# Kernel optimization log

Measured on AMD Instinct MI355X. Metric: run time of the kernel, lower is better.

## Reference

```python
import jax, jax.numpy as jnp
import numpy as np

COMPRESSION = 2

def setup_inputs() -> dict:
    key = jax.random.key(0)
    k = jax.random.split(key, 5)
    B, H, W, C, Ci = 8, 56, 56, 256, 128
    return {
        "x": jax.random.normal(k[0], (B, H, W, C), dtype=jnp.float32),
        "w_theta": jax.random.normal(k[1], (C, Ci), dtype=jnp.float32) * (2.0 / C) ** 0.5,
        "w_phi": jax.random.normal(k[2], (C, Ci), dtype=jnp.float32) * (2.0 / C) ** 0.5,
        "w_g": jax.random.normal(k[3], (C, Ci), dtype=jnp.float32) * (2.0 / C) ** 0.5,
        "w_final": jax.random.normal(k[4], (Ci, C), dtype=jnp.float32) * (2.0 / Ci) ** 0.5,
    }

def _maxpool1d(z, pool):
    # z: [B, N, Ci]; non-overlapping max pool along N (Keras MaxPool1D default stride=pool)
    B, N, Ci = z.shape
    return z[:, : (N // pool) * pool].reshape(B, N // pool, pool, Ci).max(axis=2)

def reference(x, w_theta, w_phi, w_g, w_final):
    B, H, W, C = x.shape
    Ci = w_theta.shape[1]
    N = H * W
    xf = x.reshape(B, N, C)
    # 1x1 convs == per-position matmuls
    theta = xf @ w_theta                      # [B, N, Ci]
    phi = _maxpool1d(xf @ w_phi, COMPRESSION)  # [B, N/2, Ci]
    g = _maxpool1d(xf @ w_g, COMPRESSION)      # [B, N/2, Ci]
    f = jnp.einsum('bnc,bmc->bnm', theta, phi)  # [B, N, N/2]
    f = jax.nn.softmax(f, axis=-1)
    y = jnp.einsum('bnm,bmc->bnc', f, g)        # [B, N, Ci]
    z = y @ w_final                              # [B, N, C]
    return x + z.reshape(B, H, W, C)
```

## Files before the change

### kernel.cpp

```cpp
#include <hip/hip_runtime.h>

typedef _Float16 f16x8 __attribute__((ext_vector_type(8)));
typedef _Float16 f16x4 __attribute__((ext_vector_type(4)));
typedef short s16x4 __attribute__((ext_vector_type(4)));
typedef float f32x4 __attribute__((ext_vector_type(4)));

#define MFMA_K32(a, b, c) __builtin_amdgcn_mfma_f32_16x16x32_f16(a, b, c, 0, 0, 0)
#define MFMA_BF(a, b, c)  __builtin_amdgcn_mfma_f32_16x16x16bf16_1k(a, b, c, 0, 0, 0)
#define MFMA_F16(a, b, c) __builtin_amdgcn_mfma_f32_16x16x16f16(a, b, c, 0, 0, 0)


__device__ __forceinline__ f16x8 ld8f(const float* __restrict__ p) {
    f32x4 a = *(const f32x4*)p;
    f32x4 b = *(const f32x4*)(p + 4);
    f16x8 r;
    r[0] = (_Float16)a[0]; r[1] = (_Float16)a[1];
    r[2] = (_Float16)a[2]; r[3] = (_Float16)a[3];
    r[4] = (_Float16)b[0]; r[5] = (_Float16)b[1];
    r[6] = (_Float16)b[2]; r[7] = (_Float16)b[3];
    return r;
}
__device__ __forceinline__ unsigned f2bf_rne(float f) {
    unsigned u = __float_as_uint(f);
    return (u + 0x7FFFu + ((u >> 16) & 1u)) >> 16;
}
__device__ __forceinline__ int bfpack_rtz(float lo, float hi) {
    return (int)((__float_as_uint(hi) & 0xFFFF0000u) | (__float_as_uint(lo) >> 16));
}

__global__ void k_prep(const float* __restrict__ wt, const float* __restrict__ wp,
                       const float* __restrict__ wg, const float* __restrict__ wf,
                       _Float16* __restrict__ wt_f, _Float16* __restrict__ wfT_f) {
    int i = blockIdx.x * 256 + threadIdx.x;
    int w = i >> 15, idx = i & 32767;
    if (w < 3) {
        const float* src = (w == 0) ? wt : (w == 1) ? wp : wg;
        int k = idx >> 7, n = idx & 127;
        int ct = n >> 4, tt = n & 15, kc = k >> 5, qq = (k >> 3) & 3, jj = k & 7;
        wt_f[((w * 8 + ct) * 8 + kc) * 512 + (qq * 16 + tt) * 8 + jj] = (_Float16)src[idx];
    } else {
        int k = idx >> 8, n = idx & 255;
        int ct = n >> 4, tt = n & 15;
        int kc2 = k >> 4, qq = (k >> 2) & 3, jj = k & 3;
        wfT_f[ct * 2048 + (qq * 16 + tt) * 32 + kc2 * 4 + jj] = (_Float16)wf[idx];
    }
}

__global__ __launch_bounds__(128) void k_proj(
    const float* __restrict__ x,
    const _Float16* __restrict__ wt_f,
    _Float16* __restrict__ theta_f,
    _Float16* __restrict__ phi_f,
    short* __restrict__ g_f)
{
    const int r0   = blockIdx.x * 32;
    const int wave = threadIdx.x >> 6;
    const int lane = threadIdx.x & 63;
    const int q = lane >> 4, t = lane & 15;

    const int mrow = r0 + wave * 16 + t;
    f16x8 af[8];
#pragma unroll
    for (int kc = 0; kc < 8; ++kc)
        af[kc] = ld8f(x + mrow * 256 + kc * 32 + q * 8);

    const f32x4 zero = {0.f, 0.f, 0.f, 0.f};
    f32x4 acc[3][8];
#pragma unroll
    for (int w = 0; w < 3; ++w)
#pragma unroll
        for (int ct = 0; ct < 8; ++ct) acc[w][ct] = zero;

#pragma unroll
    for (int w = 0; w < 3; ++w)
#pragma unroll
        for (int ct = 0; ct < 8; ++ct) {
            const _Float16* Wc = wt_f + ((w * 8 + ct) * 8) * 512 + lane * 8;
#pragma unroll
            for (int kc = 0; kc < 8; ++kc)
                acc[w][ct] = MFMA_K32(af[kc], *(const f16x8*)(Wc + kc * 512), acc[w][ct]);
        }

    _Float16* tb = theta_f + (blockIdx.x * 2 + wave) * 2048;
#pragma unroll
    for (int ct = 0; ct < 8; ++ct) {
        const int off = (ct >> 1) * 512 + ((ct & 1) * 2 + (t >> 3)) * 128 + (t & 7);
#pragma unroll
        for (int r = 0; r < 4; ++r)
            tb[off + (q * 4 + r) * 8] = (_Float16)acc[0][ct][r];
    }

    const int b     = blockIdx.x / 98;
    const int mIdx  = blockIdx.x % 98;
    const int chunk = mIdx >> 1;
    const int h     = mIdx & 1;
    const int ttp   = wave * 8 + q * 2;

    _Float16* pcb = phi_f + (b * 49 + chunk) * 4096;
#pragma unroll
    for (int ct = 0; ct < 8; ++ct) {
        const int kc = ct >> 1;
        const int qq = (ct & 1) * 2 + (t >> 3);
        const int j  = t & 7;
        const int off = (h * 4 + kc) * 512 + (qq * 16 + ttp) * 8 + j;
        pcb[off]     = (_Float16)fmaxf(acc[1][ct][0], acc[1][ct][1]);
        pcb[off + 8] = (_Float16)fmaxf(acc[1][ct][2], acc[1][ct][3]);
    }

    short* gcb = g_f + (b * 49 + chunk) * 4096;
    const int qv  = wave * 2 + (q >> 1);
    const int jj0 = (q & 1) * 2;
#pragma unroll
    for (int ct = 0; ct < 8; ++ct) {
        unsigned lo = f2bf_rne(fmaxf(acc[2][ct][0], acc[2][ct][1]));
        unsigned hi = f2bf_rne(fmaxf(acc[2][ct][2], acc[2][ct][3]));
        *(unsigned*)(gcb + ct * 512 + (qv * 16 + t) * 8 + h * 4 + jj0) = lo | (hi << 16);
    }
}

#define LOADKV(DST, SRC) { _Pragma("unroll") \
    for (int j = 0; j < 8; ++j) DST[j] = *(const f16x8*)((SRC) + j * 512 + lane * 8); }

#define QKSM(PH) { \
    f32x4 st0[4], st1[4]; \
    _Pragma("unroll") for (int m = 0; m < 4; ++m) { st0[m] = zero; st1[m] = zero; } \
    __builtin_amdgcn_s_setprio(1); \
    _Pragma("unroll") for (int kc = 0; kc < 4; ++kc) \
      _Pragma("unroll") for (int m = 0; m < 4; ++m) { \
        st0[m] = MFMA_K32(PH[kc],     qf[m][kc], st0[m]); \
        st1[m] = MFMA_K32(PH[4 + kc], qf[m][kc], st1[m]); } \
    __builtin_amdgcn_s_setprio(0); \
    _Pragma("unroll") for (int m = 0; m < 4; ++m) { \
      f32x4 p0, p1; \
      _Pragma("unroll") for (int r = 0; r < 4; ++r) { \
        p0[r] = exp2f(st0[m][r] * L2E - SHIFT); \
        p1[r] = exp2f(st1[m][r] * L2E - SHIFT); } \
      lsum[m] += ((p0[0] + p0[1]) + (p0[2] + p0[3])) \
               + ((p1[0] + p1[1]) + (p1[2] + p1[3])); \
      u[m][0].i2[0] = bfpack_rtz(p0[0], p0[1]); \
      u[m][0].i2[1] = bfpack_rtz(p0[2], p0[3]); \
      u[m][1].i2[0] = bfpack_rtz(p1[0], p1[1]); \
      u[m][1].i2[1] = bfpack_rtz(p1[2], p1[3]); } }

#define PV(AG) { \
    __builtin_amdgcn_s_setprio(1); \
    _Pragma("unroll") for (int ct = 0; ct < 8; ++ct) { \
      union { f16x8 f; s16x4 s[2]; } uv; uv.f = AG[ct]; \
      _Pragma("unroll") for (int m = 0; m < 4; ++m) { \
        o[m][ct] = MFMA_BF(uv.s[0], u[m][0].v, o[m][ct]); \
        o[m][ct] = MFMA_BF(uv.s[1], u[m][1].v, o[m][ct]); } } \
    __builtin_amdgcn_s_setprio(0); }

__global__ __launch_bounds__(256) void k_attn(
    const _Float16* __restrict__ theta_f,
    const _Float16* __restrict__ phi_f,
    const short* __restrict__ g_f,
    const _Float16* __restrict__ wfT_f,
    const float* __restrict__ x,
    float* __restrict__ out)
{
    const int blk  = blockIdx.x;
    const int b    = blk & 7;
    const int blkm = blk >> 3;
    const int wave = threadIdx.x >> 6;
    const int lane = threadIdx.x & 63;
    const int q = lane >> 4, t = lane & 15;

    __shared__ __align__(16) float cbuf[2][8192];
    __shared__ float lbuf[2][256];

    const int tIdx0 = b * 196 + blkm * 4;
    const _Float16* ph = phi_f + b * 200704;
    const _Float16* gt = (const _Float16*)(g_f + b * 200704);

    f16x8 qf[4][4];
#pragma unroll
    for (int m = 0; m < 4; ++m)
#pragma unroll
        for (int kc = 0; kc < 4; ++kc)
            qf[m][kc] = *(const f16x8*)(theta_f + (tIdx0 + m) * 2048 + kc * 512 + lane * 8);

    const f32x4 zero = {0.f, 0.f, 0.f, 0.f};
    f32x4 o[4][8];
#pragma unroll
    for (int m = 0; m < 4; ++m)
#pragma unroll
        for (int ct = 0; ct < 8; ++ct) o[m][ct] = zero;
    float lsum[4] = {0.f, 0.f, 0.f, 0.f};
    union ubf { int i2[2]; s16x4 v; } u[4][2];
    const float L2E = 1.44269504f, SHIFT = 104.0f;

    f16x8 phA[8], phB[8], ag[8];
    int c = wave;
    LOADKV(phA, ph + c * 4096);

#pragma unroll 1
    for (int k = 0; k < 6; ++k) {
        LOADKV(ag, gt + c * 4096);
        QKSM(phA);
        LOADKV(phB, ph + (c + 4) * 4096);
        PV(ag);
        LOADKV(ag, gt + (c + 4) * 4096);
        QKSM(phB);
        if (c + 8 <= 48) LOADKV(phA, ph + (c + 8) * 4096);
        PV(ag);
        c += 8;
    }
    if (wave == 0) {
        LOADKV(ag, gt + 48 * 4096);
        QKSM(phA);
        PV(ag);
    }

    if (wave >= 2) {
        float* cb = cbuf[wave - 2];
#pragma unroll
        for (int m = 0; m < 4; ++m) {
#pragma unroll
            for (int ct = 0; ct < 8; ++ct)
                *(f32x4*)&cb[(m * 8 + ct) * 256 + lane * 4] = o[m][ct];
            lbuf[wave - 2][m * 64 + lane] = lsum[m];
        }
    }
    __syncthreads();
    if (wave < 2) {
        const float* cb = cbuf[wave];
#pragma unroll
        for (int m = 0; m < 4; ++m) {
#pragma unroll
            for (int ct = 0; ct < 8; ++ct)
                o[m][ct] += *(const f32x4*)&cb[(m * 8 + ct) * 256 + lane * 4];
            lsum[m] += lbuf[wave][m * 64 + lane];
        }
    }
    __syncthreads();
    if (wave == 1) {
        float* cb = cbuf[0];
#pragma unroll
        for (int m = 0; m < 4; ++m) {
#pragma unroll
            for (int ct = 0; ct < 8; ++ct)
                *(f32x4*)&cb[(m * 8 + ct) * 256 + lane * 4] = o[m][ct];
            lbuf[0][m * 64 + lane] = lsum[m];
        }
    }
    __syncthreads();
    f32x4 ow[8];
    float lw;
    if (wave == 0) {
        const float* cb = cbuf[0];
#pragma unroll
        for (int m = 0; m < 4; ++m) {
#pragma unroll
            for (int ct = 0; ct < 8; ++ct)
                o[m][ct] += *(const f32x4*)&cb[(m * 8 + ct) * 256 + lane * 4];
            lsum[m] += lbuf[0][m * 64 + lane];
        }
        float* cw = cbuf[1];
#pragma unroll
        for (int m = 1; m < 4; ++m) {
#pragma unroll
            for (int ct = 0; ct < 8; ++ct)
                *(f32x4*)&cw[((m - 1) * 8 + ct) * 256 + lane * 4] = o[m][ct];
            lbuf[1][(m - 1) * 64 + lane] = lsum[m];
        }
#pragma unroll
        for (int ct = 0; ct < 8; ++ct) ow[ct] = o[0][ct];
        lw = lsum[0];
    }
    __syncthreads();
    if (wave > 0) {
        const float* cw = cbuf[1];
#pragma unroll
        for (int ct = 0; ct < 8; ++ct)
            ow[ct] = *(const f32x4*)&cw[((wave - 1) * 8 + ct) * 256 + lane * 4];
        lw = lbuf[1][(wave - 1) * 64 + lane];
    }

    float lf = lw;
    lf += __shfl_xor(lf, 16);
    lf += __shfl_xor(lf, 32);
    const float inv = 1.0f / lf;

    f16x4 yf[8];
#pragma unroll
    for (int ct = 0; ct < 8; ++ct)
#pragma unroll
        for (int r = 0; r < 4; ++r)
            yf[ct][r] = (_Float16)(ow[ct][r] * inv);

    const int row = tIdx0 * 16 + wave * 16 + t;
#pragma unroll 1
    for (int ctile = 0; ctile < 16; ++ctile) {
        union { f16x8 v8; f16x4 v4[2]; } w[4];
#pragma unroll
        for (int p = 0; p < 4; ++p)
            w[p].v8 = *(const f16x8*)(wfT_f + ctile * 2048 + lane * 32 + p * 8);
        f32x4 acc = zero;
#pragma unroll
        for (int kc2 = 0; kc2 < 8; ++kc2)
            acc = MFMA_F16(w[kc2 >> 1].v4[kc2 & 1], yf[kc2], acc);
        const int col = ctile * 16 + q * 4;
        f32x4 xv = *(const f32x4*)(x + row * 256 + col);
        *(f32x4*)(out + row * 256 + col) = acc + xv;
    }
}

extern "C" void kernel_launch(void* const* d_in, const int* in_sizes, int n_in,
                              void* d_out, int out_size, void* d_ws, size_t ws_size,
                              hipStream_t stream) {
    const float* x  = (const float*)d_in[0];
    const float* wt = (const float*)d_in[1];
    const float* wp = (const float*)d_in[2];
    const float* wg = (const float*)d_in[3];
    const float* wf = (const float*)d_in[4];
    float* out = (float*)d_out;

    _Float16* ws      = (_Float16*)d_ws;
    _Float16* wt_f    = ws;
    _Float16* wfT_f   = ws + 98304;
    _Float16* theta_f = ws + 131072;
    _Float16* phi_f   = ws + 3342336;
    short*    g_f     = (short*)(ws + 4947968);

    k_prep<<<dim3(512), 256, 0, stream>>>(wt, wp, wg, wf, wt_f, wfT_f);
    k_proj<<<dim3(784), 128, 0, stream>>>(x, wt_f, theta_f, phi_f, g_f);
    k_attn<<<dim3(392), 256, 0, stream>>>(theta_f, phi_f, g_f, wfT_f, x, out);
}
```

Measured before the change: 166.4 us.

## Split projection per weight matrix and halve query rows per attention block

k_proj now gives each wave a single (row tile, weight) pair instead of computing all three projections per wave, which triples the wave count and cuts accumulator registers. k_attn processes 2 query tiles per block instead of 4, doubling the grid to 784 blocks. Its final reduction and output GEMM are split so each wave handles half the output columns of one query tile. The aim is more parallelism and occupancy on a 256-CU part. The cost is that each phi/g tile is reloaded twice as often and x rows are re-read and converted three times in k_proj.

Measured after the change: 173.6 us. +4.3%, slower.

```diff
diff --git a/kernel.cpp b/kernel.cpp
--- a/kernel.cpp
+++ b/kernel.cpp
@@ -46,75 +46,79 @@
     }
 }
 
-__global__ __launch_bounds__(128) void k_proj(
+__global__ __launch_bounds__(256) void k_proj(
     const float* __restrict__ x,
     const _Float16* __restrict__ wt_f,
     _Float16* __restrict__ theta_f,
     _Float16* __restrict__ phi_f,
     short* __restrict__ g_f)
 {
-    const int r0   = blockIdx.x * 32;
-    const int wave = threadIdx.x >> 6;
+    const int u    = blockIdx.x * 4 + (threadIdx.x >> 6);
     const int lane = threadIdx.x & 63;
     const int q = lane >> 4, t = lane & 15;
 
-    const int mrow = r0 + wave * 16 + t;
+    const int tt = u / 3;
+    const int w  = u - tt * 3;
+
+    const int mrow = tt * 16 + t;
     f16x8 af[8];
 #pragma unroll
     for (int kc = 0; kc < 8; ++kc)
         af[kc] = ld8f(x + mrow * 256 + kc * 32 + q * 8);
 
     const f32x4 zero = {0.f, 0.f, 0.f, 0.f};
-    f32x4 acc[3][8];
-#pragma unroll
-    for (int w = 0; w < 3; ++w)
-#pragma unroll
-        for (int ct = 0; ct < 8; ++ct) acc[w][ct] = zero;
-
-#pragma unroll
-    for (int w = 0; w < 3; ++w)
+    f32x4 acc[8];
+#pragma unroll
+    for (int ct = 0; ct < 8; ++ct) acc[ct] = zero;
+
+#pragma unroll
+    for (int ct = 0; ct < 8; ++ct) {
+        const _Float16* Wc = wt_f + ((w * 8 + ct) * 8) * 512 + lane * 8;
+#pragma unroll
+        for (int kc = 0; kc < 8; ++kc)
+            acc[ct] = MFMA_K32(af[kc], *(const f16x8*)(Wc + kc * 512), acc[ct]);
+    }
+
+    if (w == 0) {
+        _Float16* tb = theta_f + tt * 2048;
 #pragma unroll
         for (int ct = 0; ct < 8; ++ct) {
-            const _Float16* Wc = wt_f + ((w * 8 + ct) * 8) * 512 + lane * 8;
-#pragma unroll
-            for (int kc = 0; kc < 8; ++kc)
-                acc[w][ct] = MFMA_K32(af[kc], *(const f16x8*)(Wc + kc * 512), acc[w][ct]);
-        }
-
-    _Float16* tb = theta_f + (blockIdx.x * 2 + wave) * 2048;
-#pragma unroll
-    for (int ct = 0; ct < 8; ++ct) {
-        const int off = (ct >> 1) * 512 + ((ct & 1) * 2 + (t >> 3)) * 128 + (t & 7);
-#pragma unroll
-        for (int r = 0; r < 4; ++r)
-            tb[off + (q * 4 + r) * 8] = (_Float16)acc[0][ct][r];
-    }
-
-    const int b     = blockIdx.x / 98;
-    const int mIdx  = blockIdx.x % 98;
-    const int chunk = mIdx >> 1;
-    const int h     = mIdx & 1;
-    const int ttp   = wave * 8 + q * 2;
-
-    _Float16* pcb = phi_f + (b * 49 + chunk) * 4096;
-#pragma unroll
-    for (int ct = 0; ct < 8; ++ct) {
-        const int kc = ct >> 1;
-        const int qq = (ct & 1) * 2 + (t >> 3);
-        const int j  = t & 7;
-        const int off = (h * 4 + kc) * 512 + (qq * 16 + ttp) * 8 + j;
-        pcb[off]     = (_Float16)fmaxf(acc[1][ct][0], acc[1][ct][1]);
-        pcb[off + 8] = (_Float16)fmaxf(acc[1][ct][2], acc[1][ct][3]);
-    }
-
-    short* gcb = g_f + (b * 49 + chunk) * 4096;
-    const int qv  = wave * 2 + (q >> 1);
-    const int jj0 = (q & 1) * 2;
-#pragma unroll
-    for (int ct = 0; ct < 8; ++ct) {
-        unsigned lo = f2bf_rne(fmaxf(acc[2][ct][0], acc[2][ct][1]));
-        unsigned hi = f2bf_rne(fmaxf(acc[2][ct][2], acc[2][ct][3]));
-        *(unsigned*)(gcb + ct * 512 + (qv * 16 + t) * 8 + h * 4 + jj0) = lo | (hi << 16);
+            const int off = (ct >> 1) * 512 + ((ct & 1) * 2 + (t >> 3)) * 128 + (t & 7);
+#pragma unroll
+            for (int r = 0; r < 4; ++r)
+                tb[off + (q * 4 + r) * 8] = (_Float16)acc[ct][r];
+        }
+        return;
+    }
+
+    const int b     = tt / 196;
+    const int tl    = tt - b * 196;
+    const int chunk = tl >> 2;
+    const int sub   = tl & 3;
+    const int h     = sub >> 1;
+
+    if (w == 1) {
+        const int ttp = (sub & 1) * 8 + q * 2;
+        _Float16* pcb = phi_f + (b * 49 + chunk) * 4096;
+#pragma unroll
+        for (int ct = 0; ct < 8; ++ct) {
+            const int kc = ct >> 1;
+            const int qq = (ct & 1) * 2 + (t >> 3);
+            const int j  = t & 7;
+            const int off = (h * 4 + kc) * 512 + (qq * 16 + ttp) * 8 + j;
+            pcb[off]     = (_Float16)fmaxf(acc[ct][0], acc[ct][1]);
+            pcb[off + 8] = (_Float16)fmaxf(acc[ct][2], acc[ct][3]);
+        }
+    } else {
+        short* gcb = g_f + (b * 49 + chunk) * 4096;
+        const int qv  = (sub & 1) * 2 + (q >> 1);
+        const int jj0 = (q & 1) * 2;
+#pragma unroll
+        for (int ct = 0; ct < 8; ++ct) {
+            unsigned lo = f2bf_rne(fmaxf(acc[ct][0], acc[ct][1]));
+            unsigned hi = f2bf_rne(fmaxf(acc[ct][2], acc[ct][3]));
+            *(unsigned*)(gcb + ct * 512 + (qv * 16 + t) * 8 + h * 4 + jj0) = lo | (hi << 16);
+        }
     }
 }
 
@@ -122,15 +126,15 @@
     for (int j = 0; j < 8; ++j) DST[j] = *(const f16x8*)((SRC) + j * 512 + lane * 8); }
 
 #define QKSM(PH) { \
-    f32x4 st0[4], st1[4]; \
-    _Pragma("unroll") for (int m = 0; m < 4; ++m) { st0[m] = zero; st1[m] = zero; } \
+    f32x4 st0[2], st1[2]; \
+    _Pragma("unroll") for (int m = 0; m < 2; ++m) { st0[m] = zero; st1[m] = zero; } \
     __builtin_amdgcn_s_setprio(1); \
     _Pragma("unroll") for (int kc = 0; kc < 4; ++kc) \
-      _Pragma("unroll") for (int m = 0; m < 4; ++m) { \
+      _Pragma("unroll") for (int m = 0; m < 2; ++m) { \
         st0[m] = MFMA_K32(PH[kc],     qf[m][kc], st0[m]); \
         st1[m] = MFMA_K32(PH[4 + kc], qf[m][kc], st1[m]); } \
     __builtin_amdgcn_s_setprio(0); \
-    _Pragma("unroll") for (int m = 0; m < 4; ++m) { \
+    _Pragma("unroll") for (int m = 0; m < 2; ++m) { \
       f32x4 p0, p1; \
       _Pragma("unroll") for (int r = 0; r < 4; ++r) { \
         p0[r] = exp2f(st0[m][r] * L2E - SHIFT); \
@@ -146,7 +150,7 @@
     __builtin_amdgcn_s_setprio(1); \
     _Pragma("unroll") for (int ct = 0; ct < 8; ++ct) { \
       union { f16x8 f; s16x4 s[2]; } uv; uv.f = AG[ct]; \
-      _Pragma("unroll") for (int m = 0; m < 4; ++m) { \
+      _Pragma("unroll") for (int m = 0; m < 2; ++m) { \
         o[m][ct] = MFMA_BF(uv.s[0], u[m][0].v, o[m][ct]); \
         o[m][ct] = MFMA_BF(uv.s[1], u[m][1].v, o[m][ct]); } } \
     __builtin_amdgcn_s_setprio(0); }
@@ -166,28 +170,28 @@
     const int lane = threadIdx.x & 63;
     const int q = lane >> 4, t = lane & 15;
 
-    __shared__ __align__(16) float cbuf[2][8192];
-    __shared__ float lbuf[2][256];
-
-    const int tIdx0 = b * 196 + blkm * 4;
+    __shared__ __align__(16) float cbuf[2][4096];
+    __shared__ float lbuf[2][128];
+
+    const int tIdx0 = b * 196 + blkm * 2;
     const _Float16* ph = phi_f + b * 200704;
     const _Float16* gt = (const _Float16*)(g_f + b * 200704);
 
-    f16x8 qf[4][4];
-#pragma unroll
-    for (int m = 0; m < 4; ++m)
+    f16x8 qf[2][4];
+#pragma unroll
+    for (int m = 0; m < 2; ++m)
 #pragma unroll
         for (int kc = 0; kc < 4; ++kc)
             qf[m][kc] = *(const f16x8*)(theta_f + (tIdx0 + m) * 2048 + kc * 512 + lane * 8);
 
     const f32x4 zero = {0.f, 0.f, 0.f, 0.f};
-    f32x4 o[4][8];
-#pragma unroll
-    for (int m = 0; m < 4; ++m)
+    f32x4 o[2][8];
+#pragma unroll
+    for (int m = 0; m < 2; ++m)
 #pragma unroll
         for (int ct = 0; ct < 8; ++ct) o[m][ct] = zero;
-    float lsum[4] = {0.f, 0.f, 0.f, 0.f};
-    union ubf { int i2[2]; s16x4 v; } u[4][2];
+    float lsum[2] = {0.f, 0.f};
+    union ubf { int i2[2]; s16x4 v; } u[2][2];
     const float L2E = 1.44269504f, SHIFT = 104.0f;
 
     f16x8 phA[8], phB[8], ag[8];
@@ -215,7 +219,7 @@
     if (wave >= 2) {
         float* cb = cbuf[wave - 2];
 #pragma unroll
-        for (int m = 0; m < 4; ++m) {
+        for (int m = 0; m < 2; ++m) {
 #pragma unroll
             for (int ct = 0; ct < 8; ++ct)
                 *(f32x4*)&cb[(m * 8 + ct) * 256 + lane * 4] = o[m][ct];
@@ -226,7 +230,7 @@
     if (wave < 2) {
         const float* cb = cbuf[wave];
 #pragma unroll
-        for (int m = 0; m < 4; ++m) {
+        for (int m = 0; m < 2; ++m) {
 #pragma unroll
             for (int ct = 0; ct < 8; ++ct)
                 o[m][ct] += *(const f32x4*)&cb[(m * 8 + ct) * 256 + lane * 4];
@@ -237,7 +241,7 @@
     if (wave == 1) {
         float* cb = cbuf[0];
 #pragma unroll
-        for (int m = 0; m < 4; ++m) {
+        for (int m = 0; m < 2; ++m) {
 #pragma unroll
             for (int ct = 0; ct < 8; ++ct)
                 *(f32x4*)&cb[(m * 8 + ct) * 256 + lane * 4] = o[m][ct];
@@ -245,39 +249,31 @@
         }
     }
     __syncthreads();
-    f32x4 ow[8];
-    float lw;
     if (wave == 0) {
         const float* cb = cbuf[0];
 #pragma unroll
-        for (int m = 0; m < 4; ++m) {
+        for (int m = 0; m < 2; ++m) {
 #pragma unroll
             for (int ct = 0; ct < 8; ++ct)
                 o[m][ct] += *(const f32x4*)&cb[(m * 8 + ct) * 256 + lane * 4];
             lsum[m] += lbuf[0][m * 64 + lane];
         }
-        float* cw = cbuf[1];
-#pragma unroll
-        for (int m = 1; m < 4; ++m) {
-#pragma unroll
-            for (int ct = 0; ct < 8; ++ct)
-                *(f32x4*)&cw[((m - 1) * 8 + ct) * 256 + lane * 4] = o[m][ct];
-            lbuf[1][(m - 1) * 64 + lane] = lsum[m];
-        }
-#pragma unroll
-        for (int ct = 0; ct < 8; ++ct) ow[ct] = o[0][ct];
-        lw = lsum[0];
+#pragma unroll
+        for (int m = 0; m < 2; ++m) {
+#pragma unroll
+            for (int ct = 0; ct < 8; ++ct)
+                *(f32x4*)&cbuf[m][ct * 256 + lane * 4] = o[m][ct];
+            lbuf[m][lane] = lsum[m];
+        }
     }
     __syncthreads();
-    if (wave > 0) {
-        const float* cw = cbuf[1];
-#pragma unroll
-        for (int ct = 0; ct < 8; ++ct)
-            ow[ct] = *(const f32x4*)&cw[((wave - 1) * 8 + ct) * 256 + lane * 4];
-        lw = lbuf[1][(wave - 1) * 64 + lane];
-    }
-
-    float lf = lw;
+
+    const int mt = wave & 1;
+    f32x4 ow[8];
+#pragma unroll
+    for (int ct = 0; ct < 8; ++ct)
+        ow[ct] = *(const f32x4*)&cbuf[mt][ct * 256 + lane * 4];
+    float lf = lbuf[mt][lane];
     lf += __shfl_xor(lf, 16);
     lf += __shfl_xor(lf, 32);
     const float inv = 1.0f / lf;
@@ -289,9 +285,11 @@
         for (int r = 0; r < 4; ++r)
             yf[ct][r] = (_Float16)(ow[ct][r] * inv);
 
-    const int row = tIdx0 * 16 + wave * 16 + t;
+    const int row = (tIdx0 + mt) * 16 + t;
+    const int c0  = (wave >> 1) * 8;
 #pragma unroll 1
-    for (int ctile = 0; ctile < 16; ++ctile) {
+    for (int ci = 0; ci < 8; ++ci) {
+        const int ctile = c0 + ci;
         union { f16x8 v8; f16x4 v4[2]; } w[4];
 #pragma unroll
         for (int p = 0; p < 4; ++p)
@@ -323,7 +321,7 @@
     _Float16* phi_f   = ws + 3342336;
     short*    g_f     = (short*)(ws + 4947968);
 
-    k_prep<<<dim3(512), 256, 0, stream>>>(wt, wp, wg, wf, wt_f, wfT_f);
-    k_proj<<<dim3(784), 128, 0, stream>>>(x, wt_f, theta_f, phi_f, g_f);
-    k_attn<<<dim3(392), 256, 0, stream>>>(theta_f, phi_f, g_f, wfT_f, x, out);
-}
+    k_prep<<<dim3(512),  256, 0, stream>>>(wt, wp, wg, wf, wt_f, wfT_f);
+    k_proj<<<dim3(1176), 256, 0, stream>>>(x, wt_f, theta_f, phi_f, g_f);
+    k_attn<<<dim3(784),  256, 0, stream>>>(theta_f, phi_f, g_f, wfT_f, x, out);
+}
```
